# Kernel tuning notes

Measured on AMD Instinct MI355X. Metric: run time of the kernel, lower is better.

Reference implementation:

```python
import jax, jax.numpy as jnp
import numpy as np

N, E, G = 50000, 800000, 512          # nodes, edges, graphs in batch
DIN, DH, H, DOUT = 128, 128, 2, 128   # dim_in, dim_h, heads, dim_out
NEG_SLOPE = 0.2
EPS_BN = 1e-5


def setup_inputs():
    key = jax.random.key(0)
    ks = jax.random.split(key, 12)
    def glorot(k, shape, fan):
        return (jax.random.normal(k, shape, jnp.float32) / np.float32(np.sqrt(fan)))
    return dict(
        x=jax.random.normal(ks[0], (N, DIN), jnp.float32),
        edge_index=jax.random.randint(ks[1], (2, E), 0, N, dtype=jnp.int32),
        batch=jnp.sort(jax.random.randint(ks[2], (N,), 0, G, dtype=jnp.int32)),
        Wl1=glorot(ks[3], (DIN, H * DH), DIN),
        Wr1=glorot(ks[4], (DIN, H * DH), DIN),
        att1=glorot(ks[5], (H, DH), DH),
        b1=jnp.zeros((H * DH,), jnp.float32),
        gamma=jnp.ones((H * DH,), jnp.float32),
        beta=jnp.zeros((H * DH,), jnp.float32),
        Wl2=glorot(ks[6], (H * DH, DOUT), H * DH),
        Wr2=glorot(ks[7], (H * DH, DOUT), H * DH),
        att2=glorot(ks[8], (1, DOUT), DOUT),
        b2=jnp.zeros((DOUT,), jnp.float32),
        Wlin=glorot(ks[9], (DOUT, 2), DOUT),
        blin=jnp.zeros((2,), jnp.float32),
    )


def gatv2_conv(x, src, dst, Wl, Wr, att, bias, heads, dh, n):
    # x: [n, F]; src/dst: [Etot] (self-loops already appended)
    xl = (x @ Wl).reshape(n, heads, dh)  # source transform (messages)
    xr = (x @ Wr).reshape(n, heads, dh)  # target transform
    m = xl[src] + xr[dst]                             # [Etot, H, dh]
    e = jnp.einsum('ehd,hd->eh', jax.nn.leaky_relu(m, NEG_SLOPE), att)  # [Etot, H]
    # softmax over incoming edges of each target node
    emax = jax.ops.segment_max(e, dst, num_segments=n)
    ex = jnp.exp(e - emax[dst])
    denom = jax.ops.segment_sum(ex, dst, num_segments=n)
    alpha = ex / (denom[dst] + 1e-16)                 # [Etot, H]
    out = jax.ops.segment_sum(xl[src] * alpha[:, :, None], dst, num_segments=n)
    return out.reshape(n, heads * dh) + bias


def reference(x, edge_index, batch, Wl1, Wr1, att1, b1, gamma, beta,
              Wl2, Wr2, att2, b2, Wlin, blin):
    loops = jnp.arange(N, dtype=edge_index.dtype)
    src = jnp.concatenate([edge_index[0], loops])
    dst = jnp.concatenate([edge_index[1], loops])

    h = gatv2_conv(x, src, dst, Wl1, Wr1, att1, b1, H, DH, N)   # [N, H*DH]
    h = jax.nn.elu(h)
    # BatchNorm over node dimension (training-mode batch stats)
    mu = h.mean(axis=0)
    var = h.var(axis=0)
    h = (h - mu) * jax.lax.rsqrt(var + EPS_BN) * gamma + beta
    # dropout p=0 -> identity
    h = gatv2_conv(h, src, dst, Wl2, Wr2, att2, b2, 1, DOUT, N)  # [N, DOUT]

    # global mean pool per graph
    s = jax.ops.segment_sum(h, batch, num_segments=G)
    cnt = jax.ops.segment_sum(jnp.ones((N,), h.dtype), batch, num_segments=G)
    pooled = s / jnp.maximum(cnt, 1.0)[:, None]                  # [G, DOUT]
    return pooled @ Wlin + blin                                  # [G, 2]
```

## Files before the change

kernel.cpp:

```cpp
#include <hip/hip_runtime.h>


#define DIN 128
#define F1 256
#define F2 128
#define NEG_SLOPE 0.2f

typedef unsigned short u16;
typedef __attribute__((ext_vector_type(8))) short short8;
typedef __attribute__((ext_vector_type(4))) float floatx4;
typedef __attribute__((ext_vector_type(2))) float f32x2;

__device__ __forceinline__ float bf2f(u16 u) {
  return __uint_as_float(((unsigned int)u) << 16);
}
__device__ __forceinline__ u16 f2bf(float f) {
  unsigned int x = __float_as_uint(f);
  return (u16)((x + 0x7fffu + ((x >> 16) & 1u)) >> 16);
}
__device__ __forceinline__ void load8(const u16* p, float (&f)[8]) {
  short8 v = *(const short8*)p;
#pragma unroll
  for (int k = 0; k < 8; k++) f[k] = bf2f((u16)v[k]);
}

__device__ __forceinline__ f32x2 bf2x(unsigned int u) {
  f32x2 r;
  r.x = __uint_as_float(u << 16);
  r.y = __uint_as_float(u & 0xffff0000u);
  return r;
}
__device__ __forceinline__ f32x2 pk_add(f32x2 a, f32x2 b) {
  f32x2 d;
  asm("v_pk_add_f32 %0, %1, %2" : "=v"(d) : "v"(a), "v"(b));
  return d;
}
__device__ __forceinline__ f32x2 pk_fma(f32x2 a, f32x2 b, f32x2 c) {
  f32x2 d;
  asm("v_pk_fma_f32 %0, %1, %2, %3" : "=v"(d) : "v"(a), "v"(b), "v"(c));
  return d;
}
__device__ __forceinline__ f32x2 pk_abs(f32x2 a) {
  f32x2 r;
  r.x = __uint_as_float(__float_as_uint(a.x) & 0x7fffffffu);
  r.y = __uint_as_float(__float_as_uint(a.y) & 0x7fffffffu);
  return r;
}

template <int CTRL>
__device__ __forceinline__ float dppadd(float s) {
  int t = __builtin_amdgcn_update_dpp(0, __float_as_int(s), CTRL, 0xF, 0xF, false);
  return s + __int_as_float(t);
}

struct PTab { const void* src[8]; int off[9]; };
__global__ __launch_bounds__(256) void k_convert_all(
    const void* __restrict__ xsrc, u16* __restrict__ xb, int n4, int nxb,
    PTab t, u16* __restrict__ pb, int ptotal, int npb,
    const void* __restrict__ Wl1s, const void* __restrict__ Wr1s,
    const void* __restrict__ Wl2s, const void* __restrict__ Wr2s,
    u16* __restrict__ Wl1t, u16* __restrict__ Wr1t,
    u16* __restrict__ Wl2t, u16* __restrict__ Wr2t,
    int* __restrict__ zbase, int zn, int* __restrict__ flag) {
  __shared__ int flagS;
  int tid = threadIdx.x;
  if (tid < 64) {
    int cnt = 0;
#pragma unroll
    for (int i = 0; i < 2; ++i) {
      u16 v = ((const u16*)xsrc)[2 * (tid + 64 * i)];
      int e = (v >> 7) & 0xFF;
      if (e >= 115 && e <= 130) cnt++;
    }
#pragma unroll
    for (int m = 1; m <= 32; m <<= 1) cnt += __shfl_xor(cnt, m, 64);
    if (tid == 0) flagS = (cnt < 64) ? 1 : 0;
  }
  __syncthreads();
  const int fl = flagS;
  if (blockIdx.x == 0 && tid == 0) *flag = fl;

  int b = blockIdx.x;
  if (b < nxb) {
    int i = b * 256 + tid;
    if (i >= n4) return;
    if (fl) {
      float4 a = ((const float4*)xsrc)[i];
      ushort4 o;
      o.x = f2bf(a.x); o.y = f2bf(a.y); o.z = f2bf(a.z); o.w = f2bf(a.w);
      ((ushort4*)xb)[i] = o;
    } else {
      ((ulong1*)xb)[i] = ((const ulong1*)xsrc)[i];
    }
    return;
  }
  b -= nxb;
  if (b < npb) {
    int i = b * 256 + tid;
    if (i >= ptotal) return;
    int s = 0;
#pragma unroll
    for (int k = 1; k < 8; k++) s += (i >= t.off[k]);
    int local = i - t.off[s];
    pb[i] = fl ? f2bf(((const float*)t.src[s])[local]) : ((const u16*)t.src[s])[local];
    return;
  }
  b -= npb;
  if (b < 512) {
    int seg = b >> 7;
    int i = (b & 127) * 256 + tid;
    const void* s; u16* d; int NL, sh;
    if      (seg == 0) { s = Wl1s; d = Wl1t; NL = 256; sh = 7; }
    else if (seg == 1) { s = Wr1s; d = Wr1t; NL = 256; sh = 7; }
    else if (seg == 2) { s = Wl2s; d = Wl2t; NL = 128; sh = 8; }
    else               { s = Wr2s; d = Wr2t; NL = 128; sh = 8; }
    int n = i >> sh, k = i & ((1 << sh) - 1);
    int si = k * NL + n;
    d[i] = fl ? f2bf(((const float*)s)[si]) : ((const u16*)s)[si];
    return;
  }
  b -= 512;
  int i = b * 256 + tid;
  if (i < zn) zbase[i] = 0;
}

__global__ void k_hist(const int* __restrict__ ei, int* __restrict__ hist,
                       int E, int Etot) {
  int e = blockIdx.x * 256 + threadIdx.x;
  if (e >= Etot) return;
  int dst = (e < E) ? ei[E + e] : (e - E);
  atomicAdd(&hist[dst], 1);
}

__global__ __launch_bounds__(256) void k_scan(
    const int* __restrict__ hist, int* __restrict__ rowptr,
    int* __restrict__ cursor, int n, int Etot) {
  __shared__ int tmp[256];
  __shared__ int wsum[4];
  const int t = threadIdx.x;
  const int base = blockIdx.x * 256;

  int pre = 0;
  const int4* h4 = (const int4*)hist;
  const int n4 = base >> 2;
  for (int i = t; i < n4; i += 256) {
    int4 v = h4[i];
    pre += v.x + v.y + v.z + v.w;
  }
#pragma unroll
  for (int m = 1; m <= 32; m <<= 1) pre += __shfl_xor(pre, m, 64);
  if ((t & 63) == 0) wsum[t >> 6] = pre;
  __syncthreads();
  const int off = wsum[0] + wsum[1] + wsum[2] + wsum[3];

  const int gid = base + t;
  int v = (gid < n) ? hist[gid] : 0;
  tmp[t] = v;
  __syncthreads();
  for (int o = 1; o < 256; o <<= 1) {
    int add = (t >= o) ? tmp[t - o] : 0;
    __syncthreads();
    tmp[t] += add;
    __syncthreads();
  }
  if (gid < n) {
    int ex = off + tmp[t] - v;
    rowptr[gid] = ex;
    cursor[gid] = ex;
  }
  if (gid == 0) rowptr[n] = Etot;
}

__global__ void k_scatter(const int* __restrict__ ei, int* __restrict__ cursor,
                          int* __restrict__ ssrc, int E, int Etot) {
  int e = blockIdx.x * 256 + threadIdx.x;
  if (e >= Etot) return;
  int src, dst;
  if (e < E) { src = ei[e]; dst = ei[E + e]; }
  else       { src = e - E; dst = e - E; }
  int pos = atomicAdd(&cursor[dst], 1);
  ssrc[pos] = src;
}

template<int K, bool RB>
__global__ __launch_bounds__(256) void k_gemm(
    const u16* __restrict__ A, const u16* __restrict__ Blt, const u16* __restrict__ Brt,
    int NL, u16* __restrict__ Cl, u16* __restrict__ Cr, int M,
    const float* __restrict__ rbias) {
  const int tid = threadIdx.x;
  const int m0 = blockIdx.x * 64;
  const int n0g = blockIdx.y * 64;
  const u16* Bt; u16* C; int col0;
  if (n0g < NL) { Bt = Blt; C = Cl; col0 = n0g; }
  else          { Bt = Brt; C = Cr; col0 = n0g - NL; }

  const int wave = tid >> 6, lane = tid & 63;
  const int wm = wave >> 1, wn = wave & 1;
  const int quad = lane >> 4, l16 = lane & 15;

  floatx4 acc[2][2] = {};
#pragma unroll
  for (int k0 = 0; k0 < K; k0 += 32) {
    short8 af[2], bfr[2];
#pragma unroll
    for (int mt = 0; mt < 2; mt++) {
      int row = m0 + wm * 32 + mt * 16 + l16;
      if (row > M - 1) row = M - 1;
      af[mt] = *(const short8*)(A + (size_t)row * K + k0 + quad * 8);
    }
#pragma unroll
    for (int nt = 0; nt < 2; nt++) {
      int nn = col0 + wn * 32 + nt * 16 + l16;
      bfr[nt] = *(const short8*)(Bt + (size_t)nn * K + k0 + quad * 8);
    }
#pragma unroll
    for (int mt = 0; mt < 2; mt++)
#pragma unroll
      for (int nt = 0; nt < 2; nt++)
        acc[mt][nt] = __builtin_amdgcn_mfma_f32_16x16x32_bf16(af[mt], bfr[nt], acc[mt][nt], 0, 0, 0);
  }

#pragma unroll
  for (int mt = 0; mt < 2; mt++)
#pragma unroll
    for (int nt = 0; nt < 2; nt++) {
      float rb = 0.f;
      if (RB) rb = rbias[n0g + wn * 32 + nt * 16 + l16];
#pragma unroll
      for (int r = 0; r < 4; r++) {
        int row = m0 + wm * 32 + mt * 16 + quad * 4 + r;
        if (row < M) {
          int col = col0 + wn * 32 + nt * 16 + l16;
          C[(size_t)row * NL + col] = f2bf(acc[mt][nt][r] + rb);
        }
      }
    }
}

template<int CPL, int MODE>
__global__ __launch_bounds__(256) void k_agg(
    const u16* __restrict__ xl, const u16* __restrict__ xr,
    const u16* __restrict__ att, const u16* __restrict__ bias,
    const int* __restrict__ rowptr, const int* __restrict__ ssrc,
    void* __restrict__ outv, int n) {
  constexpr int F = CPL * 16;
  constexpr int NV = CPL / 8;
  constexpr int NP = CPL / 2;
  const int wave = threadIdx.x >> 6, lane = threadIdx.x & 63;
  const int q = lane >> 4, l = lane & 15;
  const int ch0 = l * CPL;

  f32x2 a06[NP];
  {
    const unsigned int* atu = (const unsigned int*)(att + ch0);
#pragma unroll
    for (int p = 0; p < NP; p++) {
      f32x2 a = bf2x(atu[p]);
      a06[p].x = 0.6f * a.x; a06[p].y = 0.6f * a.y;
    }
  }
  f32x2 c23; c23.x = 2.0f / 3.0f; c23.y = 2.0f / 3.0f;

#pragma unroll
  for (int nd = 0; nd < 2; nd++) {
    const int node = blockIdx.x * 8 + nd * 4 + wave;
    if (node >= n) continue;

    f32x2 xr2[NP], acc2[NP];
    {
      const unsigned int* xru = (const unsigned int*)(xr + (size_t)node * F + ch0);
#pragma unroll
      for (int p = 0; p < NP; p++) {
        xr2[p] = bf2x(xru[p]);
        acc2[p].x = 0.f; acc2[p].y = 0.f;
      }
    }

    const int jb = __builtin_amdgcn_readfirstlane(rowptr[node]);
    const int je = __builtin_amdgcn_readfirstlane(rowptr[node + 1]);
    const int jec = je - 1;
    float l_run = 0.f;

    auto cidx = [&](int j) -> int { return j < jec ? j : jec; };

    uint4 bufA[NV], bufB[NV];
    auto REFILL = [&](uint4 (&buf)[NV], int srow) {
#pragma unroll
      for (int v = 0; v < NV; v++)
        buf[v] = *(const uint4*)(xl + (size_t)srow * F + ch0 + v * 8);
    };

    auto SLOT = [&](uint4 (&buf)[NV], int jbase) {
      f32x2 xl2[NP];
      f32x2 s2; s2.x = 0.f; s2.y = 0.f;
#pragma unroll
      for (int v = 0; v < NV; v++) {
        unsigned int dw[4] = {buf[v].x, buf[v].y, buf[v].z, buf[v].w};
#pragma unroll
        for (int k = 0; k < 4; k++) {
          const int p = v * 4 + k;
          f32x2 xv = bf2x(dw[k]);
          f32x2 m  = pk_add(xv, xr2[p]);
          f32x2 am = pk_abs(m);
          f32x2 t  = pk_fma(am, c23, m);
          s2 = pk_fma(a06[p], t, s2);
          xl2[p] = xv;
        }
      }
      float s = s2.x + s2.y;
      s = dppadd<0xB1>(s);
      s = dppadd<0x4E>(s);
      s = dppadd<0x141>(s);
      if (CPL == 8) s = dppadd<0x140>(s);
      float pe = (jbase + q < je) ? __expf(fminf(s, 80.f)) : 0.f;
      l_run += pe;
      f32x2 p2; p2.x = pe; p2.y = pe;
#pragma unroll
      for (int p = 0; p < NP; p++) acc2[p] = pk_fma(p2, xl2[p], acc2[p]);
    };

    REFILL(bufA, ssrc[cidx(jb + q)]);
    REFILL(bufB, ssrc[cidx(jb + 4 + q)]);
    int sA2 = ssrc[cidx(jb + 8 + q)];
    int sB2 = ssrc[cidx(jb + 12 + q)];

    int j = jb;
    for (; j + 4 < je; j += 8) {
      SLOT(bufA, j);
      REFILL(bufA, sA2);
      SLOT(bufB, j + 4);
      REFILL(bufB, sB2);
      sA2 = ssrc[cidx(j + 16 + q)];
      sB2 = ssrc[cidx(j + 20 + q)];
    }
    if (j < je) SLOT(bufA, j);

#pragma unroll
    for (int p = 0; p < NP; p++) {
      acc2[p].x += __shfl_xor(acc2[p].x, 16, 64);
      acc2[p].x += __shfl_xor(acc2[p].x, 32, 64);
      acc2[p].y += __shfl_xor(acc2[p].y, 16, 64);
      acc2[p].y += __shfl_xor(acc2[p].y, 32, 64);
    }
    l_run += __shfl_xor(l_run, 16, 64);
    l_run += __shfl_xor(l_run, 32, 64);

    if (q == 0) {
      float inv = 1.f / (l_run + 1e-16f);
      const unsigned int* bu = (const unsigned int*)(bias + ch0);
      if (MODE == 0) {
#pragma unroll
        for (int v = 0; v < NV; v++) {
          short8 o;
#pragma unroll
          for (int k = 0; k < 4; k++) {
            const int p = v * 4 + k;
            f32x2 b = bf2x(bu[p]);
            float t0 = acc2[p].x * inv + b.x;
            float t1 = acc2[p].y * inv + b.y;
            t0 = t0 > 0.f ? t0 : (__expf(t0) - 1.f);
            t1 = t1 > 0.f ? t1 : (__expf(t1) - 1.f);
            o[k * 2]     = (short)f2bf(t0);
            o[k * 2 + 1] = (short)f2bf(t1);
          }
          *(short8*)((u16*)outv + (size_t)node * F + ch0 + v * 8) = o;
        }
      } else {
#pragma unroll
        for (int v = 0; v < NV; v++) {
          float w[8];
#pragma unroll
          for (int k = 0; k < 4; k++) {
            const int p = v * 4 + k;
            f32x2 b = bf2x(bu[p]);
            w[k * 2]     = acc2[p].x * inv + b.x;
            w[k * 2 + 1] = acc2[p].y * inv + b.y;
          }
          float* op = (float*)outv + (size_t)node * F + ch0 + v * 8;
          *(float4*)op = make_float4(w[0], w[1], w[2], w[3]);
          *(float4*)(op + 4) = make_float4(w[4], w[5], w[6], w[7]);
        }
      }
    }
  }
}

__global__ __launch_bounds__(256) void k_stats(
    const u16* __restrict__ h, float* __restrict__ gsum,
    float* __restrict__ gsumsq, int n) {
  __shared__ float smS[8][256], smQ[8][256];
  int t = threadIdx.x;
  int rg = t >> 5, cl = t & 31;
  int ch0 = cl * 8;
  float s[8] = {}, q[8] = {};
  for (int r = blockIdx.x * 8 + rg; r < n; r += gridDim.x * 8) {
    float v[8];
    load8(h + (size_t)r * F1 + ch0, v);
#pragma unroll
    for (int k = 0; k < 8; k++) { s[k] += v[k]; q[k] += v[k] * v[k]; }
  }
#pragma unroll
  for (int k = 0; k < 8; k++) { smS[rg][ch0 + k] = s[k]; smQ[rg][ch0 + k] = q[k]; }
  __syncthreads();
  float ts = 0.f, tq = 0.f;
#pragma unroll
  for (int g = 0; g < 8; g++) { ts += smS[g][t]; tq += smQ[g][t]; }
  atomicAdd(&gsum[t], ts);
  atomicAdd(&gsumsq[t], tq);
}

__global__ __launch_bounds__(256) void k_foldbn(
    const float* __restrict__ gsum, const float* __restrict__ gsumsq,
    const u16* __restrict__ gamma, const u16* __restrict__ beta,
    u16* __restrict__ Wl2t, u16* __restrict__ Wr2t,
    float* __restrict__ rbias, float invn) {
  __shared__ float red[8];
  int t = threadIdx.x, n = blockIdx.x;
  float mu = gsum[t] * invn;
  float var = gsumsq[t] * invn - mu * mu;
  float a = bf2f(gamma[t]) * rsqrtf(fmaxf(var, 0.f) + 1e-5f);
  float b = bf2f(beta[t]) - mu * a;
  float wl = bf2f(Wl2t[n * 256 + t]);
  float wr = bf2f(Wr2t[n * 256 + t]);
  float sl = b * wl, sr = b * wr;
  Wl2t[n * 256 + t] = f2bf(a * wl);
  Wr2t[n * 256 + t] = f2bf(a * wr);
#pragma unroll
  for (int m = 1; m <= 32; m <<= 1) {
    sl += __shfl_xor(sl, m, 64);
    sr += __shfl_xor(sr, m, 64);
  }
  int wave = t >> 6, lane = t & 63;
  if (lane == 0) { red[wave] = sl; red[4 + wave] = sr; }
  __syncthreads();
  if (t == 0) rbias[n] = red[0] + red[1] + red[2] + red[3];
  if (t == 1) rbias[128 + n] = red[4] + red[5] + red[6] + red[7];
}

__device__ __forceinline__ int lowerb(const int* __restrict__ a, int n, int key) {
  int lo = 0, hi = n;
  while (lo < hi) { int m = (lo + hi) >> 1; if (a[m] < key) lo = m + 1; else hi = m; }
  return lo;
}

__global__ __launch_bounds__(256) void k_poolfinal(
    const float* __restrict__ h2, const int* __restrict__ batch,
    const u16* __restrict__ Wlin, const u16* __restrict__ blin,
    void* __restrict__ out, const int* __restrict__ flag, int G, int N) {
  __shared__ float sm[4][128];
  int g = blockIdx.x;
  int wave = threadIdx.x >> 6, lane = threadIdx.x & 63;
  int jb = lowerb(batch, N, g);
  int je = lowerb(batch, N, g + 1);
  int ch = lane * 2;
  float c0 = 0.f, c1 = 0.f;
  for (int r = jb + wave; r < je; r += 4) {
    float2 v = *(const float2*)(h2 + (size_t)r * F2 + ch);
    c0 += v.x; c1 += v.y;
  }
  sm[wave][ch] = c0;
  sm[wave][ch + 1] = c1;
  __syncthreads();
  if (wave == 0) {
    c0 = sm[0][ch] + sm[1][ch] + sm[2][ch] + sm[3][ch];
    c1 = sm[0][ch + 1] + sm[1][ch + 1] + sm[2][ch + 1] + sm[3][ch + 1];
    float cf = fmaxf((float)(je - jb), 1.f);
    c0 /= cf; c1 /= cf;
    float s0 = c0 * bf2f(Wlin[ch * 2 + 0]) + c1 * bf2f(Wlin[(ch + 1) * 2 + 0]);
    float s1 = c0 * bf2f(Wlin[ch * 2 + 1]) + c1 * bf2f(Wlin[(ch + 1) * 2 + 1]);
#pragma unroll
    for (int m = 1; m <= 32; m <<= 1) {
      s0 += __shfl_xor(s0, m, 64);
      s1 += __shfl_xor(s1, m, 64);
    }
    if (lane == 0) {
      float o0 = s0 + bf2f(blin[0]);
      float o1 = s1 + bf2f(blin[1]);
      if (*flag) {
        ((float*)out)[g * 2 + 0] = o0;
        ((float*)out)[g * 2 + 1] = o1;
      } else {
        ((u16*)out)[g * 2 + 0] = f2bf(o0);
        ((u16*)out)[g * 2 + 1] = f2bf(o1);
      }
    }
  }
}

extern "C" void kernel_launch(void* const* d_in, const int* in_sizes, int n_in,
                              void* d_out, int out_size, void* d_ws, size_t ws_size,
                              hipStream_t stream) {
  const int* ei    = (const int*)d_in[1];
  const int* batch = (const int*)d_in[2];

  const int N = in_sizes[0] / DIN;
  const int E = in_sizes[1] / 2;
  const int G = out_size / 2;
  const int Etot = E + N;

  char* p = (char*)d_ws;
  auto alloc = [&](size_t bytes) {
    char* r = p;
    p += (bytes + 255) & ~(size_t)255;
    return r;
  };
  int*  flag     = (int*)alloc(256);
  int*  hist     = (int*)alloc((size_t)N * 4);
  float* gsum    = (float*)alloc(1024);
  float* gsumsq  = (float*)alloc(1024);
  int   zn       = (int)(((char*)gsumsq + 1024) - (char*)hist) / 4;
  int*  rowptr   = (int*)alloc((size_t)(N + 1) * 4);
  int*  cursor   = (int*)alloc((size_t)N * 4);
  float* rbias   = (float*)alloc(256 * 4);
  int*  ssrc     = (int*)alloc((size_t)Etot * 4);
  u16*  xb       = (u16*)alloc((size_t)N * DIN * 2);
  u16*  pb       = (u16*)alloc(4096);
  u16*  Wl1t     = (u16*)alloc(DIN * F1 * 2);
  u16*  Wr1t     = (u16*)alloc(DIN * F1 * 2);
  u16*  Wl2t     = (u16*)alloc(F1 * F2 * 2);
  u16*  Wr2t     = (u16*)alloc(F1 * F2 * 2);
  u16*  regionA  = (u16*)alloc((size_t)N * F1 * 2);
  u16*  regionB  = (u16*)alloc((size_t)N * F1 * 2);
  u16*  regionC  = (u16*)alloc((size_t)N * F1 * 2);

  u16*  xl1  = regionA;
  u16*  xr1  = regionB;
  u16*  helu = regionC;
  u16*  xl2  = regionB;
  u16*  xr2  = regionB + (size_t)N * F2;
  float* h2  = (float*)regionA;

  const int pidx[8] = {5, 6, 7, 8, 11, 12, 13, 14};
  PTab tab;
  int accum = 0;
  for (int i = 0; i < 8; i++) {
    tab.src[i] = d_in[pidx[i]];
    tab.off[i] = accum;
    accum += in_sizes[pidx[i]];
  }
  tab.off[8] = accum;
  int n4 = in_sizes[0] / 4;
  int nxb = (n4 + 255) / 256;
  int npb = (accum + 255) / 256;
  int nzb = (zn + 255) / 256;
  k_convert_all<<<nxb + npb + 512 + nzb, 256, 0, stream>>>(
      d_in[0], xb, n4, nxb, tab, pb, accum, npb,
      d_in[3], d_in[4], d_in[9], d_in[10], Wl1t, Wr1t, Wl2t, Wr2t,
      hist, zn, flag);
  u16 *pAtt1 = pb + tab.off[0], *pB1 = pb + tab.off[1], *pGamma = pb + tab.off[2],
      *pBeta = pb + tab.off[3], *pAtt2 = pb + tab.off[4], *pB2 = pb + tab.off[5],
      *pWlin = pb + tab.off[6], *pBlin = pb + tab.off[7];

  const int eb = (Etot + 255) / 256;
  const int sb = (N + 255) / 256;

  k_hist<<<eb, 256, 0, stream>>>(ei, hist, E, Etot);
  k_scan<<<sb, 256, 0, stream>>>(hist, rowptr, cursor, N, Etot);
  k_scatter<<<eb, 256, 0, stream>>>(ei, cursor, ssrc, E, Etot);

  dim3 g1((N + 63) / 64, (2 * F1) / 64);
  k_gemm<DIN, false><<<g1, 256, 0, stream>>>(xb, Wl1t, Wr1t, F1, xl1, xr1, N, nullptr);

  k_agg<16, 0><<<(N + 7) / 8, 256, 0, stream>>>(xl1, xr1, pAtt1, pB1, rowptr, ssrc, helu, N);

  k_stats<<<256, 256, 0, stream>>>(helu, gsum, gsumsq, N);
  k_foldbn<<<128, 256, 0, stream>>>(gsum, gsumsq, pGamma, pBeta, Wl2t, Wr2t, rbias,
                                    1.0f / (float)N);

  dim3 g2((N + 63) / 64, (2 * F2) / 64);
  k_gemm<F1, true><<<g2, 256, 0, stream>>>(helu, Wl2t, Wr2t, F2, xl2, xr2, N, rbias);

  k_agg<8, 1><<<(N + 7) / 8, 256, 0, stream>>>(xl2, xr2, pAtt2, pB2, rowptr, ssrc, h2, N);

  k_poolfinal<<<G, 256, 0, stream>>>(h2, batch, pWlin, pBlin, d_out, flag, G, N);
}
```

Baseline: 438.7 us.

## Fold histogram into convert kernel and regroup layer-2 aggregation lanes

The edge-destination histogram moves into the combined conversion kernel as extra blocks, and the zeroing of hist becomes a separate memset. This removes one kernel launch. The aggregation kernel gains a lanes-per-group parameter. Layer 2 now uses 8 lanes with 16 channels each, so 8 edges are handled per wave step instead of 4, which raises memory-level parallelism on gathers. The risk is a race: the histogram atomics run in the same grid as other blocks, so they depend on the memset finishing first. It also costs more registers per lane in layer 2.

```diff
diff --git a/kernel.cpp b/kernel.cpp
--- a/kernel.cpp
+++ b/kernel.cpp
@@ -61,7 +61,8 @@
     const void* __restrict__ Wl2s, const void* __restrict__ Wr2s,
     u16* __restrict__ Wl1t, u16* __restrict__ Wr1t,
     u16* __restrict__ Wl2t, u16* __restrict__ Wr2t,
-    int* __restrict__ zbase, int zn, int* __restrict__ flag) {
+    int* __restrict__ zbase, int zn, int nzb, int* __restrict__ flag,
+    const int* __restrict__ ei, int* __restrict__ hist, int E, int Etot) {
   __shared__ int flagS;
   int tid = threadIdx.x;
   if (tid < 64) {
@@ -120,16 +121,19 @@
     return;
   }
   b -= 512;
-  int i = b * 256 + tid;
-  if (i < zn) zbase[i] = 0;
-}
-
-__global__ void k_hist(const int* __restrict__ ei, int* __restrict__ hist,
-                       int E, int Etot) {
-  int e = blockIdx.x * 256 + threadIdx.x;
-  if (e >= Etot) return;
-  int dst = (e < E) ? ei[E + e] : (e - E);
-  atomicAdd(&hist[dst], 1);
+  if (b < nzb) {
+    int i = b * 256 + tid;
+    if (i < zn) zbase[i] = 0;
+    return;
+  }
+  b -= nzb;
+  {
+    int e = b * 256 + tid;
+    if (e < Etot) {
+      int dst = (e < E) ? ei[E + e] : (e - E);
+      atomicAdd(&hist[dst], 1);
+    }
+  }
 }
 
 __global__ __launch_bounds__(256) void k_scan(
@@ -237,18 +241,19 @@
     }
 }
 
-template<int CPL, int MODE>
+template<int CPL, int LPG, int MODE>
 __global__ __launch_bounds__(256) void k_agg(
     const u16* __restrict__ xl, const u16* __restrict__ xr,
     const u16* __restrict__ att, const u16* __restrict__ bias,
     const int* __restrict__ rowptr, const int* __restrict__ ssrc,
     void* __restrict__ outv, int n) {
-  constexpr int F = CPL * 16;
+  constexpr int F = CPL * LPG;
+  constexpr int GPW = 64 / LPG;
   constexpr int NV = CPL / 8;
   constexpr int NP = CPL / 2;
   const int wave = threadIdx.x >> 6, lane = threadIdx.x & 63;
-  const int q = lane >> 4, l = lane & 15;
-  const int ch0 = l * CPL;
+  const int g = lane / LPG, lg = lane % LPG;
+  const int ch0 = lg * CPL;
 
   f32x2 a06[NP];
   {
@@ -311,41 +316,41 @@
       s = dppadd<0xB1>(s);
       s = dppadd<0x4E>(s);
       s = dppadd<0x141>(s);
-      if (CPL == 8) s = dppadd<0x140>(s);
-      float pe = (jbase + q < je) ? __expf(fminf(s, 80.f)) : 0.f;
+      float pe = (jbase + g < je) ? __expf(fminf(s, 80.f)) : 0.f;
       l_run += pe;
       f32x2 p2; p2.x = pe; p2.y = pe;
 #pragma unroll
       for (int p = 0; p < NP; p++) acc2[p] = pk_fma(p2, xl2[p], acc2[p]);
     };
 
-    REFILL(bufA, ssrc[cidx(jb + q)]);
-    REFILL(bufB, ssrc[cidx(jb + 4 + q)]);
-    int sA2 = ssrc[cidx(jb + 8 + q)];
-    int sB2 = ssrc[cidx(jb + 12 + q)];
+    REFILL(bufA, ssrc[cidx(jb + g)]);
+    REFILL(bufB, ssrc[cidx(jb + GPW + g)]);
+    int sA2 = ssrc[cidx(jb + 2 * GPW + g)];
+    int sB2 = ssrc[cidx(jb + 3 * GPW + g)];
 
     int j = jb;
-    for (; j + 4 < je; j += 8) {
+    for (; j + GPW < je; j += 2 * GPW) {
       SLOT(bufA, j);
       REFILL(bufA, sA2);
-      SLOT(bufB, j + 4);
+      SLOT(bufB, j + GPW);
       REFILL(bufB, sB2);
-      sA2 = ssrc[cidx(j + 16 + q)];
-      sB2 = ssrc[cidx(j + 20 + q)];
+      sA2 = ssrc[cidx(j + 4 * GPW + g)];
+      sB2 = ssrc[cidx(j + 5 * GPW + g)];
     }
     if (j < je) SLOT(bufA, j);
 
 #pragma unroll
     for (int p = 0; p < NP; p++) {
-      acc2[p].x += __shfl_xor(acc2[p].x, 16, 64);
-      acc2[p].x += __shfl_xor(acc2[p].x, 32, 64);
-      acc2[p].y += __shfl_xor(acc2[p].y, 16, 64);
-      acc2[p].y += __shfl_xor(acc2[p].y, 32, 64);
-    }
-    l_run += __shfl_xor(l_run, 16, 64);
-    l_run += __shfl_xor(l_run, 32, 64);
-
-    if (q == 0) {
+#pragma unroll
+      for (int m = LPG; m <= 32; m <<= 1) {
+        acc2[p].x += __shfl_xor(acc2[p].x, m, 64);
+        acc2[p].y += __shfl_xor(acc2[p].y, m, 64);
+      }
+    }
+#pragma unroll
+    for (int m = LPG; m <= 32; m <<= 1) l_run += __shfl_xor(l_run, m, 64);
+
+    if (lane < LPG) {
       float inv = 1.f / (l_run + 1e-16f);
       const unsigned int* bu = (const unsigned int*)(bias + ch0);
       if (MODE == 0) {
@@ -508,7 +513,7 @@
   int*  hist     = (int*)alloc((size_t)N * 4);
   float* gsum    = (float*)alloc(1024);
   float* gsumsq  = (float*)alloc(1024);
-  int   zn       = (int)(((char*)gsumsq + 1024) - (char*)hist) / 4;
+  int   zn       = (int)(((char*)gsumsq + 1024) - (char*)gsum) / 4;
   int*  rowptr   = (int*)alloc((size_t)(N + 1) * 4);
   int*  cursor   = (int*)alloc((size_t)N * 4);
   float* rbias   = (float*)alloc(256 * 4);
@@ -530,6 +535,8 @@
   u16*  xr2  = regionB + (size_t)N * F2;
   float* h2  = (float*)regionA;
 
+  hipMemsetAsync(hist, 0, (size_t)N * 4, stream);
+
   const int pidx[8] = {5, 6, 7, 8, 11, 12, 13, 14};
   PTab tab;
   int accum = 0;
@@ -543,25 +550,24 @@
   int nxb = (n4 + 255) / 256;
   int npb = (accum + 255) / 256;
   int nzb = (zn + 255) / 256;
-  k_convert_all<<<nxb + npb + 512 + nzb, 256, 0, stream>>>(
+  const int eb = (Etot + 255) / 256;
+  k_convert_all<<<nxb + npb + 512 + nzb + eb, 256, 0, stream>>>(
       d_in[0], xb, n4, nxb, tab, pb, accum, npb,
       d_in[3], d_in[4], d_in[9], d_in[10], Wl1t, Wr1t, Wl2t, Wr2t,
-      hist, zn, flag);
+      (int*)gsum, zn, nzb, flag, ei, hist, E, Etot);
   u16 *pAtt1 = pb + tab.off[0], *pB1 = pb + tab.off[1], *pGamma = pb + tab.off[2],
       *pBeta = pb + tab.off[3], *pAtt2 = pb + tab.off[4], *pB2 = pb + tab.off[5],
       *pWlin = pb + tab.off[6], *pBlin = pb + tab.off[7];
 
-  const int eb = (Etot + 255) / 256;
   const int sb = (N + 255) / 256;
 
-  k_hist<<<eb, 256, 0, stream>>>(ei, hist, E, Etot);
   k_scan<<<sb, 256, 0, stream>>>(hist, rowptr, cursor, N, Etot);
   k_scatter<<<eb, 256, 0, stream>>>(ei, cursor, ssrc, E, Etot);
 
   dim3 g1((N + 63) / 64, (2 * F1) / 64);
   k_gemm<DIN, false><<<g1, 256, 0, stream>>>(xb, Wl1t, Wr1t, F1, xl1, xr1, N, nullptr);
 
-  k_agg<16, 0><<<(N + 7) / 8, 256, 0, stream>>>(xl1, xr1, pAtt1, pB1, rowptr, ssrc, helu, N);
+  k_agg<16, 16, 0><<<(N + 7) / 8, 256, 0, stream>>>(xl1, xr1, pAtt1, pB1, rowptr, ssrc, helu, N);
 
   k_stats<<<256, 256, 0, stream>>>(helu, gsum, gsumsq, N);
   k_foldbn<<<128, 256, 0, stream>>>(gsum, gsumsq, pGamma, pBeta, Wl2t, Wr2t, rbias,
@@ -570,7 +576,7 @@
   dim3 g2((N + 63) / 64, (2 * F2) / 64);
   k_gemm<F1, true><<<g2, 256, 0, stream>>>(helu, Wl2t, Wr2t, F2, xl2, xr2, N, rbias);
 
-  k_agg<8, 1><<<(N + 7) / 8, 256, 0, stream>>>(xl2, xr2, pAtt2, pB2, rowptr, ssrc, h2, N);
+  k_agg<16, 8, 1><<<(N + 7) / 8, 256, 0, stream>>>(xl2, xr2, pAtt2, pB2, rowptr, ssrc, h2, N);
 
   k_poolfinal<<<G, 256, 0, stream>>>(h2, batch, pWlin, pBlin, d_out, flag, G, N);
 }
```

Result: no change. 441.1 us (+0.5%).
